# Performance work log

Hardware: AMD Instinct MI355X
Metric: run time of the kernel (lower is better)

Reference implementation:

```python
import jax, jax.numpy as jnp
import numpy as np

B, S, DM, H = 4, 2048, 768, 12
HD = DM // H
HEAD_Z = float(np.sqrt(HD))


def norm_layer(x, scale, bias):
    # custom normalization over last dim: (x - mean)/std * scale + bias, scalar scale/bias, no eps
    mean = x.mean(axis=2, keepdims=True)
    std = jnp.sqrt(((x - mean) ** 2).mean(axis=2, keepdims=True))
    return (x - mean) / std * scale + bias


def setup_inputs() -> dict:
    key = jax.random.key(0)
    ks = jax.random.split(key, 12)
    s = 1.0 / np.sqrt(DM)
    return {
        "base": jax.random.normal(ks[0], (B, S, DM), dtype=jnp.float32),
        "Wqkv": jax.random.normal(ks[1], (DM, 3 * DM), dtype=jnp.float32) * s,
        "bqkv": jax.random.normal(ks[2], (3 * DM,), dtype=jnp.float32) * s,
        "W1": jax.random.normal(ks[3], (DM, DM), dtype=jnp.float32) * s,
        "b1": jax.random.normal(ks[4], (DM,), dtype=jnp.float32) * s,
        "W2": jax.random.normal(ks[5], (DM, DM), dtype=jnp.float32) * s,
        "b2": jax.random.normal(ks[6], (DM,), dtype=jnp.float32) * s,
        "n1_scale": jax.random.uniform(ks[7], (1,), jnp.float32, -s, s) + 0.5,
        "n1_bias": jax.random.uniform(ks[8], (1,), jnp.float32, -s, s),
        "n2_scale": jax.random.uniform(ks[9], (1,), jnp.float32, -s, s) + 0.5,
        "n2_bias": jax.random.uniform(ks[10], (1,), jnp.float32, -s, s),
    }


def reference(base, Wqkv, bqkv, W1, b1, W2, b2, n1_scale, n1_bias, n2_scale, n2_bias):
    qkv = base @ Wqkv + bqkv                     # [B,S,3*DM]
    q, k, v = jnp.split(qkv, 3, axis=2)
    # per-head attention, vectorized over heads: the torch loop with broadcast-mul-sum
    # is mathematically softmax(QK^T/sqrt(hd)) @ V per head
    q = q.reshape(B, S, H, HD)
    k = k.reshape(B, S, H, HD)
    v = v.reshape(B, S, H, HD)
    scores = jnp.einsum('bqhd,bkhd->bhqk', q, k) / HEAD_Z  # [B,H,S,S]
    attn = jax.nn.softmax(scores, axis=-1)
    av = jnp.einsum('bhqk,bkhd->bqhd', attn, v).reshape(B, S, DM)
    hidden = norm_layer(av @ W1 + b1 + base, n1_scale, n1_bias)
    out = norm_layer(jax.nn.relu(hidden @ W2 + b2) + hidden, n2_scale, n2_bias)
    return out
```

## Files before the change

kernel.cpp:

```cpp
#include <hip/hip_runtime.h>
#include <hip/hip_bf16.h>
#include <stdint.h>

#define B_ 4
#define S_ 2048
#define DM_ 768
#define H_ 12
#define HD_ 64
#define ROWS (B_*S_)
#define QKVN (3*DM_)

typedef __attribute__((ext_vector_type(8))) short short8;
typedef __attribute__((ext_vector_type(4))) float floatx4;
typedef __attribute__((ext_vector_type(8))) unsigned short ushort8;
typedef __attribute__((ext_vector_type(4))) unsigned short ushort4v;
typedef __attribute__((ext_vector_type(4))) float float4_t;

__device__ __forceinline__ unsigned short f2b(float f) {
  union { float f; uint32_t u; } x; x.f = f;
  uint32_t r = x.u + 0x7FFFu + ((x.u >> 16) & 1u);
  return (unsigned short)(r >> 16);
}
__device__ __forceinline__ float b2f(unsigned short u) {
  union { uint32_t u; float f; } x; x.u = ((uint32_t)u) << 16; return x.f;
}
__device__ __forceinline__ uint32_t fbits(float f) {
  union { float f; uint32_t u; } x; x.f = f; return x.u;
}

__device__ __forceinline__ void load_lds16(const void* g, void* l) {
  __builtin_amdgcn_global_load_lds(
      (const __attribute__((address_space(1))) uint32_t*)g,
      (__attribute__((address_space(3))) uint32_t*)l, 16, 0, 0);
}

#define CVT_B 6144
#define WQ_B 1728
#define W1_B 576
__global__ __launch_bounds__(256) void prep(
    const float* __restrict__ base, unsigned short* __restrict__ base_bf,
    const float* __restrict__ Wqkv, unsigned short* __restrict__ Wqkvt,
    const float* __restrict__ W1, unsigned short* __restrict__ W1t,
    const float* __restrict__ W2, unsigned short* __restrict__ W2t) {
  __shared__ float t[32][33];
  int bid = blockIdx.x;
  int tid = threadIdx.x;
  if (bid < CVT_B) {
    int i = bid * 256 + tid;
    float4_t v = ((const float4_t*)base)[i];
    ushort4v o;
    o[0] = f2b(v[0]); o[1] = f2b(v[1]); o[2] = f2b(v[2]); o[3] = f2b(v[3]);
    ((ushort4v*)base_bf)[i] = o;
    return;
  }
  const float* W; unsigned short* Wt; int N, rel;
  if (bid < CVT_B + WQ_B)      { W = Wqkv; Wt = Wqkvt; N = QKVN; rel = bid - CVT_B; }
  else if (bid < CVT_B + WQ_B + W1_B) { W = W1; Wt = W1t; N = DM_; rel = bid - CVT_B - WQ_B; }
  else                          { W = W2; Wt = W2t; N = DM_; rel = bid - CVT_B - WQ_B - W1_B; }
  int K = DM_;
  int n0 = (rel % (N / 32)) * 32, k0 = (rel / (N / 32)) * 32;
  int tx = tid & 31, ty = tid >> 5;
#pragma unroll
  for (int i = 0; i < 4; i++)
    t[ty + i * 8][tx] = W[(size_t)(k0 + ty + i * 8) * N + n0 + tx];
  __syncthreads();
#pragma unroll
  for (int i = 0; i < 4; i++)
    Wt[(size_t)(n0 + ty + i * 8) * K + k0 + tx] = f2b(t[tx][ty + i * 8]);
}

__global__ __launch_bounds__(256, 2) void gemm_qkv(
    const unsigned short* __restrict__ A,
    const unsigned short* __restrict__ Bt,
    const float* __restrict__ bias,
    unsigned short* __restrict__ Cout,
    unsigned short* __restrict__ Vt,
    int M, int N, int K) {
  __shared__ __align__(16) unsigned short LDSbuf[2 * 128 * 128];
  unsigned short* As = LDSbuf;
  unsigned short* Bs = LDSbuf + 128 * 128;
  int tid = threadIdx.x;
  int wave = tid >> 6, lane = tid & 63;
  int quad = lane >> 4, l16 = lane & 15;
  int sr4 = lane >> 4;
  int c16 = lane & 15;
  int flat = blockIdx.x;
  int xcd = flat & 7, widx = flat >> 3;
  int mb = xcd * 8 + (widx & 7);
  int nb = widx >> 3;
  int m0 = mb * 128, n0 = nb * 128;
  int wm = (wave >> 1) * 64, wn = (wave & 1) * 64;
  floatx4 acc[4][4] = {};

  for (int kb = 0; kb < K; kb += 128) {
#pragma unroll
    for (int i = 0; i < 8; i++) {
      int op = wave * 8 + i;
      int srow = op * 4 + sr4;
      int sc = c16 ^ (srow & 15);
      load_lds16(A + (size_t)(m0 + srow) * K + kb + sc * 8, (char*)As + op * 1024);
    }
#pragma unroll
    for (int i = 0; i < 8; i++) {
      int op = wave * 8 + i;
      int srow = op * 4 + sr4;
      int sc = c16 ^ (srow & 15);
      load_lds16(Bt + (size_t)(n0 + srow) * K + kb + sc * 8, (char*)Bs + op * 1024);
    }
    __syncthreads();
#pragma unroll
    for (int ks = 0; ks < 4; ks++) {
      short8 af[4], bfr[4];
#pragma unroll
      for (int mt = 0; mt < 4; mt++)
        af[mt] = *(const short8*)(As + (wm + mt * 16 + l16) * 128 + ((ks * 4 + quad) ^ l16) * 8);
#pragma unroll
      for (int nt = 0; nt < 4; nt++)
        bfr[nt] = *(const short8*)(Bs + (wn + nt * 16 + l16) * 128 + ((ks * 4 + quad) ^ l16) * 8);
#pragma unroll
      for (int mt = 0; mt < 4; mt++)
#pragma unroll
        for (int nt = 0; nt < 4; nt++)
          acc[mt][nt] = __builtin_amdgcn_mfma_f32_16x16x32_bf16(af[mt], bfr[nt], acc[mt][nt], 0, 0, 0);
    }
    __syncthreads();
  }

  if (n0 < 2 * DM_) {
#pragma unroll
    for (int mt = 0; mt < 4; mt++) {
#pragma unroll
      for (int nt = 0; nt < 4; nt++) {
#pragma unroll
        for (int r = 0; r < 4; r++) {
          int row = m0 + wm + mt * 16 + quad * 4 + r;
          int col = n0 + wn + nt * 16 + l16;
          float v = acc[mt][nt][r] + bias[col];
          if (col < DM_) v *= 0.18033688011112042f;
          Cout[(size_t)row * N + col] = f2b(v);
        }
      }
    }
  } else {
    unsigned short* scr = LDSbuf + wave * 4608;
    int h = (n0 + wn - 2 * DM_) >> 6;
    int b = m0 >> 11;
    int s_base = (m0 & (S_ - 1)) + wm;
#pragma unroll
    for (int nt = 0; nt < 4; nt++) {
      float bv = bias[n0 + wn + nt * 16 + l16];
      ushort8 v0, v1;
#pragma unroll
      for (int j = 0; j < 8; j++) {
        v0[j] = f2b(acc[j & 3][nt][j >> 2] + bv);
        v1[j] = f2b(acc[j & 3][nt][2 + (j >> 2)] + bv);
      }
      *(ushort8*)(scr + (nt * 16 + l16) * 72 + quad * 16) = v0;
      *(ushort8*)(scr + (nt * 16 + l16) * 72 + quad * 16 + 8) = v1;
    }
#pragma unroll
    for (int it = 0; it < 8; it++) {
      int d = it * 8 + (lane >> 3);
      int ch = lane & 7;
      ushort8 w = *(const ushort8*)(scr + d * 72 + ch * 8);
      *(ushort8*)(Vt + ((size_t)(b * H_ + h) * 64 + d) * S_ + s_base + ch * 8) = w;
    }
  }
}

template <int EPI>
__global__ __launch_bounds__(256, 4) void gemm64(
    const unsigned short* __restrict__ A,
    const unsigned short* __restrict__ Bt,
    const float* __restrict__ bias,
    const unsigned short* __restrict__ res,
    unsigned short* __restrict__ Cout,
    int M, int N, int K) {
  __shared__ __align__(16) unsigned short As[64 * 64];
  __shared__ __align__(16) unsigned short Bs[128 * 64];
  int tid = threadIdx.x;
  int wave = tid >> 6, lane = tid & 63;
  int quad = lane >> 4, l16 = lane & 15;
  int e = l16 & 7;
  int sr = lane >> 3;
  int sc = (lane & 7) ^ (sr & 7);
  int flat = blockIdx.x;
  int xcd = flat & 7, widx = flat >> 3;
  int mb = xcd * 16 + (widx & 15);
  int nb = widx >> 4;
  int m0 = mb * 64, n0 = nb * 128;
  int wm = (wave >> 1) * 32, wn = (wave & 1) * 64;
  floatx4 acc[2][4] = {};

  for (int kb = 0; kb < K; kb += 64) {
#pragma unroll
    for (int i = 0; i < 2; i++) {
      int op = wave * 2 + i;
      load_lds16(A + (size_t)(m0 + op * 8 + sr) * K + kb + sc * 8, (char*)As + op * 1024);
    }
#pragma unroll
    for (int i = 0; i < 4; i++) {
      int op = wave * 4 + i;
      load_lds16(Bt + (size_t)(n0 + op * 8 + sr) * K + kb + sc * 8, (char*)Bs + op * 1024);
    }
    __syncthreads();
#pragma unroll
    for (int ks = 0; ks < 2; ks++) {
      short8 af[2], bfr[4];
#pragma unroll
      for (int mt = 0; mt < 2; mt++)
        af[mt] = *(const short8*)(As + (wm + mt * 16 + l16) * 64 + ((ks * 4 + quad) ^ e) * 8);
#pragma unroll
      for (int nt = 0; nt < 4; nt++)
        bfr[nt] = *(const short8*)(Bs + (wn + nt * 16 + l16) * 64 + ((ks * 4 + quad) ^ e) * 8);
#pragma unroll
      for (int mt = 0; mt < 2; mt++)
#pragma unroll
        for (int nt = 0; nt < 4; nt++)
          acc[mt][nt] = __builtin_amdgcn_mfma_f32_16x16x32_bf16(af[mt], bfr[nt], acc[mt][nt], 0, 0, 0);
    }
    __syncthreads();
  }
#pragma unroll
  for (int mt = 0; mt < 2; mt++) {
#pragma unroll
    for (int nt = 0; nt < 4; nt++) {
#pragma unroll
      for (int r = 0; r < 4; r++) {
        int row = m0 + wm + mt * 16 + quad * 4 + r;
        int col = n0 + wn + nt * 16 + l16;
        size_t idx = (size_t)row * N + col;
        float v = acc[mt][nt][r] + bias[col];
        if (EPI == 2) v = fmaxf(v, 0.0f);
        v += b2f(res[idx]);
        Cout[idx] = f2b(v);
      }
    }
  }
}

__global__ __launch_bounds__(256, 3) void attn(
    const unsigned short* __restrict__ qkv,
    const unsigned short* __restrict__ Vt,
    unsigned short* __restrict__ av) {
  int flat = blockIdx.x;
  int widx = (flat & 7) * 96 + (flat >> 3);
  int qt = widx & 15;
  int bh = widx >> 4;
  int b = bh / H_, h = bh % H_;
  int row0 = b * S_ + qt * 128;
  __shared__ __align__(16) unsigned short Ks[2][64 * 64];
  __shared__ __align__(16) unsigned short Vs[2][64 * 64];
  __shared__ __align__(16) unsigned short Ps[4][32 * 72];
  int tid = threadIdx.x;
  int wave = tid >> 6, lane = tid & 63;
  int quad = lane >> 4, l16 = lane & 15;
  int e = l16 & 7;
  int sr = lane >> 3;
  int sc = (lane & 7) ^ (sr & 7);

#pragma unroll
  for (int i = 0; i < 4; i++) {
    load_lds16(qkv + (size_t)(row0 + wave * 32 + i * 8 + sr) * QKVN + h * HD_ + sc * 8,
               (char*)Ps[wave] + i * 1024);
  }
  const unsigned short* kp = qkv + (size_t)(b * S_ + wave * 16 + sr) * QKVN + DM_ + h * HD_ + sc * 8;
  const unsigned short* vp = Vt + ((size_t)bh * 64 + wave * 16 + sr) * S_ + sc * 8;
  auto stageKV = [&](const unsigned short* kq, const unsigned short* vq, int buf) {
#pragma unroll
    for (int i = 0; i < 2; i++) {
      load_lds16(kq + (size_t)i * 8 * QKVN, (char*)Ks[buf] + wave * 2048 + i * 1024);
      load_lds16(vq + (size_t)i * 8 * S_, (char*)Vs[buf] + wave * 2048 + i * 1024);
    }
  };
  stageKV(kp, vp, 0);

  floatx4 accO[2][4] = {};
  floatx4 accL[2] = {};
  short8 ones;
#pragma unroll
  for (int j = 0; j < 8; j++) ones[j] = (short)0x3F80;
  __syncthreads();

  short8 qf[2][2];
#pragma unroll
  for (int mf = 0; mf < 2; mf++)
#pragma unroll
    for (int ks = 0; ks < 2; ks++)
      qf[mf][ks] = *(const short8*)(Ps[wave] + (mf * 16 + l16) * 64 + ((ks * 4 + quad) ^ e) * 8);

  int cur = 0;
  for (int kt = 0; kt < 32; kt++) {
    floatx4 sv[2][4] = {};
    __builtin_amdgcn_s_setprio(1);
#pragma unroll
    for (int ks = 0; ks < 2; ks++)
#pragma unroll
      for (int nt = 0; nt < 4; nt++) {
        short8 kf = *(const short8*)(Ks[cur] + (nt * 16 + l16) * 64 + ((ks * 4 + quad) ^ e) * 8);
#pragma unroll
        for (int mf = 0; mf < 2; mf++)
          sv[mf][nt] = __builtin_amdgcn_mfma_f32_16x16x32_bf16(qf[mf][ks], kf, sv[mf][nt], 0, 0, 0);
      }
    __builtin_amdgcn_s_setprio(0);
    if (kt + 1 < 32) {
      kp += 64 * QKVN;
      vp += 64;
      stageKV(kp, vp, cur ^ 1);
    }
#pragma unroll
    for (int mf = 0; mf < 2; mf++)
#pragma unroll
      for (int r = 0; r < 4; r++) {
        uint32_t u0 = fbits(__builtin_amdgcn_exp2f(sv[mf][0][r]));
        uint32_t u1 = fbits(__builtin_amdgcn_exp2f(sv[mf][1][r]));
        uint32_t u2 = fbits(__builtin_amdgcn_exp2f(sv[mf][2][r]));
        uint32_t u3 = fbits(__builtin_amdgcn_exp2f(sv[mf][3][r]));
        uint2 val;
        val.x = __builtin_amdgcn_perm(u1, u0, 0x07060302u);
        val.y = __builtin_amdgcn_perm(u3, u2, 0x07060302u);
        *(uint2*)(&Ps[wave][(mf * 16 + quad * 4 + r) * 72 + l16 * 4]) = val;
      }
    __builtin_amdgcn_s_setprio(1);
#pragma unroll
    for (int ks = 0; ks < 2; ks++) {
      short8 pf[2];
#pragma unroll
      for (int mf = 0; mf < 2; mf++) {
        pf[mf] = *(const short8*)(Ps[wave] + (mf * 16 + l16) * 72 + ks * 32 + quad * 8);
        accL[mf] = __builtin_amdgcn_mfma_f32_16x16x32_bf16(pf[mf], ones, accL[mf], 0, 0, 0);
      }
#pragma unroll
      for (int nt = 0; nt < 4; nt++) {
        short8 vf = *(const short8*)(Vs[cur] + (nt * 16 + l16) * 64 + ((ks * 4 + quad) ^ e) * 8);
#pragma unroll
        for (int mf = 0; mf < 2; mf++)
          accO[mf][nt] = __builtin_amdgcn_mfma_f32_16x16x32_bf16(pf[mf], vf, accO[mf][nt], 0, 0, 0);
      }
    }
    __builtin_amdgcn_s_setprio(0);
    __syncthreads();
    cur ^= 1;
  }
#pragma unroll
  for (int mf = 0; mf < 2; mf++)
#pragma unroll
    for (int r = 0; r < 4; r++) {
      float inv = 1.0f / accL[mf][r];
      int row = row0 + wave * 32 + mf * 16 + quad * 4 + r;
#pragma unroll
      for (int nt = 0; nt < 4; nt++)
        av[(size_t)row * DM_ + h * HD_ + nt * 16 + l16] = f2b(accO[mf][nt][r] * inv);
    }
}

template <int WB>
__global__ __launch_bounds__(256) void normk(
    const unsigned short* __restrict__ X, const float* __restrict__ scale,
    const float* __restrict__ bias, float* __restrict__ Y,
    unsigned short* __restrict__ Ybf) {
  int row = blockIdx.x;
  const unsigned short* x = X + (size_t)row * DM_;
  int tid = threadIdx.x;
  int wave = tid >> 6, lane = tid & 63;
  float v[3];
#pragma unroll
  for (int i = 0; i < 3; i++) v[i] = b2f(x[tid + i * 256]);
  float s = v[0] + v[1] + v[2];
#pragma unroll
  for (int o = 32; o > 0; o >>= 1) s += __shfl_xor(s, o);
  __shared__ float red[4];
  if (lane == 0) red[wave] = s;
  __syncthreads();
  float mean = (red[0] + red[1] + red[2] + red[3]) * (1.0f / DM_);
  float ss = 0.0f;
#pragma unroll
  for (int i = 0; i < 3; i++) { v[i] -= mean; ss += v[i] * v[i]; }
#pragma unroll
  for (int o = 32; o > 0; o >>= 1) ss += __shfl_xor(ss, o);
  __syncthreads();
  if (lane == 0) red[wave] = ss;
  __syncthreads();
  float var = (red[0] + red[1] + red[2] + red[3]) * (1.0f / DM_);
  float rstd = rsqrtf(var);
  float sg = scale[0], bg = bias[0];
#pragma unroll
  for (int i = 0; i < 3; i++) {
    float y = v[i] * rstd * sg + bg;
    if (WB) Ybf[(size_t)row * DM_ + tid + i * 256] = f2b(y);
    else    Y[(size_t)row * DM_ + tid + i * 256] = y;
  }
}

extern "C" void kernel_launch(void* const* d_in, const int* in_sizes, int n_in,
                              void* d_out, int out_size, void* d_ws, size_t ws_size,
                              hipStream_t stream) {
  const float* base = (const float*)d_in[0];
  const float* Wqkv = (const float*)d_in[1];
  const float* bqkv = (const float*)d_in[2];
  const float* W1 = (const float*)d_in[3];
  const float* b1 = (const float*)d_in[4];
  const float* W2 = (const float*)d_in[5];
  const float* b2 = (const float*)d_in[6];
  const float* n1s = (const float*)d_in[7];
  const float* n1b = (const float*)d_in[8];
  const float* n2s = (const float*)d_in[9];
  const float* n2b = (const float*)d_in[10];
  float* out = (float*)d_out;

  char* ws = (char*)d_ws;
  size_t off = 0;
  auto alloc = [&](size_t bytes) {
    char* p = ws + off;
    off = (off + bytes + 255) & ~(size_t)255;
    return p;
  };
  unsigned short* base_bf = (unsigned short*)alloc((size_t)ROWS * DM_ * 2);
  unsigned short* Wqkvt = (unsigned short*)alloc((size_t)QKVN * DM_ * 2);
  unsigned short* W1t = (unsigned short*)alloc((size_t)DM_ * DM_ * 2);
  unsigned short* W2t = (unsigned short*)alloc((size_t)DM_ * DM_ * 2);
  unsigned short* qkvb = (unsigned short*)alloc((size_t)ROWS * QKVN * 2);
  unsigned short* Vtb = (unsigned short*)alloc((size_t)B_ * H_ * HD_ * S_ * 2);
  unsigned short* avb = (unsigned short*)alloc((size_t)ROWS * DM_ * 2);
  unsigned short* t1b = (unsigned short*)alloc((size_t)ROWS * DM_ * 2);
  unsigned short* hbf = (unsigned short*)alloc((size_t)ROWS * DM_ * 2);

  prep<<<CVT_B + WQ_B + 2 * W1_B, 256, 0, stream>>>(
      base, base_bf, Wqkv, Wqkvt, W1, W1t, W2, W2t);
  gemm_qkv<<<dim3((QKVN / 128) * (ROWS / 128)), 256, 0, stream>>>(
      base_bf, Wqkvt, bqkv, qkvb, Vtb, ROWS, QKVN, DM_);
  attn<<<dim3((S_ / 128) * (B_ * H_)), 256, 0, stream>>>(qkvb, Vtb, avb);
  gemm64<1><<<dim3((DM_ / 128) * (ROWS / 64)), 256, 0, stream>>>(
      avb, W1t, b1, base_bf, t1b, ROWS, DM_, DM_);
  normk<1><<<ROWS, 256, 0, stream>>>(t1b, n1s, n1b, nullptr, hbf);
  gemm64<2><<<dim3((DM_ / 128) * (ROWS / 64)), 256, 0, stream>>>(
      hbf, W2t, b2, hbf, t1b, ROWS, DM_, DM_);
  normk<0><<<ROWS, 256, 0, stream>>>(t1b, n2s, n2b, out, nullptr);
}
```

Baseline: 244.5 us.

## Restructure attention to 32x32x16 MFMA with register-resident P and row sums

The attention kernel switches from 16x16x32 MFMAs to 32x32x16 MFMAs and computes S^T = K·Q^T, so that each lane's exponentiated scores can be packed straight into the B operand of the PV MFMA. This removes the LDS round-trip for P and the extra MFMA against a ones vector for the row sums; the sums are now accumulated with scalar adds plus one cross-half shuffle. Q is loaded directly into registers, and a hardware packed bf16 convert replaces the manual bit tricks. The output is staged through LDS for coalesced 16-byte stores, and the QKV epilogue's V-transpose staging is reordered to use 8-byte writes. This relies on the scale already being folded into Q, and the new register layout must match the 32x32 operand mapping exactly.

```diff
diff --git a/kernel.cpp b/kernel.cpp
--- a/kernel.cpp
+++ b/kernel.cpp
@@ -12,9 +12,11 @@
 
 typedef __attribute__((ext_vector_type(8))) short short8;
 typedef __attribute__((ext_vector_type(4))) float floatx4;
+typedef __attribute__((ext_vector_type(16))) float floatx16;
 typedef __attribute__((ext_vector_type(8))) unsigned short ushort8;
 typedef __attribute__((ext_vector_type(4))) unsigned short ushort4v;
 typedef __attribute__((ext_vector_type(4))) float float4_t;
+typedef __attribute__((ext_vector_type(4))) unsigned int uintx4;
 
 __device__ __forceinline__ unsigned short f2b(float f) {
   union { float f; uint32_t u; } x; x.f = f;
@@ -24,14 +26,16 @@
 __device__ __forceinline__ float b2f(unsigned short u) {
   union { uint32_t u; float f; } x; x.u = ((uint32_t)u) << 16; return x.f;
 }
-__device__ __forceinline__ uint32_t fbits(float f) {
-  union { float f; uint32_t u; } x; x.f = f; return x.u;
-}
 
 __device__ __forceinline__ void load_lds16(const void* g, void* l) {
   __builtin_amdgcn_global_load_lds(
       (const __attribute__((address_space(1))) uint32_t*)g,
       (__attribute__((address_space(3))) uint32_t*)l, 16, 0, 0);
+}
+__device__ __forceinline__ uint32_t cvt_pk_bf16(float a, float b) {
+  uint32_t w;
+  asm("v_cvt_pk_bf16_f32 %0, %1, %2" : "=v"(w) : "v"(a), "v"(b));
+  return w;
 }
 
 #define CVT_B 6144
@@ -146,17 +150,17 @@
     int h = (n0 + wn - 2 * DM_) >> 6;
     int b = m0 >> 11;
     int s_base = (m0 & (S_ - 1)) + wm;
+    int posq = (quad & 1) * 8 + (quad >> 1) * 4;
 #pragma unroll
     for (int nt = 0; nt < 4; nt++) {
       float bv = bias[n0 + wn + nt * 16 + l16];
-      ushort8 v0, v1;
-#pragma unroll
-      for (int j = 0; j < 8; j++) {
-        v0[j] = f2b(acc[j & 3][nt][j >> 2] + bv);
-        v1[j] = f2b(acc[j & 3][nt][2 + (j >> 2)] + bv);
+#pragma unroll
+      for (int mt = 0; mt < 4; mt++) {
+        ushort4v v;
+#pragma unroll
+        for (int r = 0; r < 4; r++) v[r] = f2b(acc[mt][nt][r] + bv);
+        *(ushort4v*)(scr + (nt * 16 + l16) * 72 + mt * 16 + posq) = v;
       }
-      *(ushort8*)(scr + (nt * 16 + l16) * 72 + quad * 16) = v0;
-      *(ushort8*)(scr + (nt * 16 + l16) * 72 + quad * 16 + 8) = v1;
     }
 #pragma unroll
     for (int it = 0; it < 8; it++) {
@@ -249,109 +253,109 @@
   int bh = widx >> 4;
   int b = bh / H_, h = bh % H_;
   int row0 = b * S_ + qt * 128;
-  __shared__ __align__(16) unsigned short Ks[2][64 * 64];
-  __shared__ __align__(16) unsigned short Vs[2][64 * 64];
-  __shared__ __align__(16) unsigned short Ps[4][32 * 72];
+  __shared__ __align__(16) unsigned short SH[4 * 64 * 64];
   int tid = threadIdx.x;
   int wave = tid >> 6, lane = tid & 63;
-  int quad = lane >> 4, l16 = lane & 15;
-  int e = l16 & 7;
+  int q = lane & 31, hi = lane >> 5;
+  int e8 = lane & 7;
   int sr = lane >> 3;
   int sc = (lane & 7) ^ (sr & 7);
 
-#pragma unroll
-  for (int i = 0; i < 4; i++) {
-    load_lds16(qkv + (size_t)(row0 + wave * 32 + i * 8 + sr) * QKVN + h * HD_ + sc * 8,
-               (char*)Ps[wave] + i * 1024);
-  }
+  const unsigned short* qrow =
+      qkv + (size_t)(row0 + wave * 32 + q) * QKVN + h * HD_ + hi * 8;
+  short8 qf[4];
+#pragma unroll
+  for (int slot = 0; slot < 4; slot++)
+    qf[slot] = *(const short8*)(qrow + slot * 16);
+
   const unsigned short* kp = qkv + (size_t)(b * S_ + wave * 16 + sr) * QKVN + DM_ + h * HD_ + sc * 8;
   const unsigned short* vp = Vt + ((size_t)bh * 64 + wave * 16 + sr) * S_ + sc * 8;
   auto stageKV = [&](const unsigned short* kq, const unsigned short* vq, int buf) {
 #pragma unroll
     for (int i = 0; i < 2; i++) {
-      load_lds16(kq + (size_t)i * 8 * QKVN, (char*)Ks[buf] + wave * 2048 + i * 1024);
-      load_lds16(vq + (size_t)i * 8 * S_, (char*)Vs[buf] + wave * 2048 + i * 1024);
+      load_lds16(kq + (size_t)i * 8 * QKVN, (char*)SH + buf * 8192 + wave * 2048 + i * 1024);
+      load_lds16(vq + (size_t)i * 8 * S_, (char*)SH + 16384 + buf * 8192 + wave * 2048 + i * 1024);
     }
   };
   stageKV(kp, vp, 0);
 
-  floatx4 accO[2][4] = {};
-  floatx4 accL[2] = {};
-  short8 ones;
-#pragma unroll
-  for (int j = 0; j < 8; j++) ones[j] = (short)0x3F80;
+  floatx16 accO[2] = {};
+  float accL = 0.0f;
   __syncthreads();
-
-  short8 qf[2][2];
-#pragma unroll
-  for (int mf = 0; mf < 2; mf++)
-#pragma unroll
-    for (int ks = 0; ks < 2; ks++)
-      qf[mf][ks] = *(const short8*)(Ps[wave] + (mf * 16 + l16) * 64 + ((ks * 4 + quad) ^ e) * 8);
 
   int cur = 0;
   for (int kt = 0; kt < 32; kt++) {
-    floatx4 sv[2][4] = {};
+    const unsigned short* Ksc = SH + cur * 4096;
+    const unsigned short* Vsc = SH + 16384 / 2 + cur * 4096;
+    floatx16 sv0 = {}, sv1 = {};
     __builtin_amdgcn_s_setprio(1);
 #pragma unroll
-    for (int ks = 0; ks < 2; ks++)
-#pragma unroll
-      for (int nt = 0; nt < 4; nt++) {
-        short8 kf = *(const short8*)(Ks[cur] + (nt * 16 + l16) * 64 + ((ks * 4 + quad) ^ e) * 8);
-#pragma unroll
-        for (int mf = 0; mf < 2; mf++)
-          sv[mf][nt] = __builtin_amdgcn_mfma_f32_16x16x32_bf16(qf[mf][ks], kf, sv[mf][nt], 0, 0, 0);
-      }
+    for (int slot = 0; slot < 4; slot++) {
+      short8 kf0 = *(const short8*)(Ksc + (q) * 64 + ((slot * 2 + hi) ^ e8) * 8);
+      short8 kf1 = *(const short8*)(Ksc + (32 + q) * 64 + ((slot * 2 + hi) ^ e8) * 8);
+      sv0 = __builtin_amdgcn_mfma_f32_32x32x16_bf16(kf0, qf[slot], sv0, 0, 0, 0);
+      sv1 = __builtin_amdgcn_mfma_f32_32x32x16_bf16(kf1, qf[slot], sv1, 0, 0, 0);
+    }
     __builtin_amdgcn_s_setprio(0);
     if (kt + 1 < 32) {
       kp += 64 * QKVN;
       vp += 64;
       stageKV(kp, vp, cur ^ 1);
     }
-#pragma unroll
-    for (int mf = 0; mf < 2; mf++)
-#pragma unroll
-      for (int r = 0; r < 4; r++) {
-        uint32_t u0 = fbits(__builtin_amdgcn_exp2f(sv[mf][0][r]));
-        uint32_t u1 = fbits(__builtin_amdgcn_exp2f(sv[mf][1][r]));
-        uint32_t u2 = fbits(__builtin_amdgcn_exp2f(sv[mf][2][r]));
-        uint32_t u3 = fbits(__builtin_amdgcn_exp2f(sv[mf][3][r]));
-        uint2 val;
-        val.x = __builtin_amdgcn_perm(u1, u0, 0x07060302u);
-        val.y = __builtin_amdgcn_perm(u3, u2, 0x07060302u);
-        *(uint2*)(&Ps[wave][(mf * 16 + quad * 4 + r) * 72 + l16 * 4]) = val;
+    uint32_t pw[4][4];
+    float psum = 0.0f;
+#pragma unroll
+    for (int s = 0; s < 4; s++) {
+#pragma unroll
+      for (int j4 = 0; j4 < 4; j4++) {
+        float a, bb;
+        if (s < 2) {
+          a = __builtin_amdgcn_exp2f(sv0[(s & 1) * 8 + 2 * j4]);
+          bb = __builtin_amdgcn_exp2f(sv0[(s & 1) * 8 + 2 * j4 + 1]);
+        } else {
+          a = __builtin_amdgcn_exp2f(sv1[(s & 1) * 8 + 2 * j4]);
+          bb = __builtin_amdgcn_exp2f(sv1[(s & 1) * 8 + 2 * j4 + 1]);
+        }
+        psum += a + bb;
+        pw[s][j4] = cvt_pk_bf16(a, bb);
       }
+    }
+    accL += psum;
     __builtin_amdgcn_s_setprio(1);
 #pragma unroll
-    for (int ks = 0; ks < 2; ks++) {
-      short8 pf[2];
-#pragma unroll
-      for (int mf = 0; mf < 2; mf++) {
-        pf[mf] = *(const short8*)(Ps[wave] + (mf * 16 + l16) * 72 + ks * 32 + quad * 8);
-        accL[mf] = __builtin_amdgcn_mfma_f32_16x16x32_bf16(pf[mf], ones, accL[mf], 0, 0, 0);
-      }
-#pragma unroll
-      for (int nt = 0; nt < 4; nt++) {
-        short8 vf = *(const short8*)(Vs[cur] + (nt * 16 + l16) * 64 + ((ks * 4 + quad) ^ e) * 8);
-#pragma unroll
-        for (int mf = 0; mf < 2; mf++)
-          accO[mf][nt] = __builtin_amdgcn_mfma_f32_16x16x32_bf16(pf[mf], vf, accO[mf][nt], 0, 0, 0);
+    for (int s = 0; s < 4; s++) {
+      uintx4 pu = {pw[s][0], pw[s][1], pw[s][2], pw[s][3]};
+      short8 pf = __builtin_bit_cast(short8, pu);
+#pragma unroll
+      for (int dt = 0; dt < 2; dt++) {
+        short8 vf = *(const short8*)(Vsc + (dt * 32 + q) * 64 + ((s * 2 + hi) ^ e8) * 8);
+        accO[dt] = __builtin_amdgcn_mfma_f32_32x32x16_bf16(vf, pf, accO[dt], 0, 0, 0);
       }
     }
     __builtin_amdgcn_s_setprio(0);
     __syncthreads();
     cur ^= 1;
   }
-#pragma unroll
-  for (int mf = 0; mf < 2; mf++)
-#pragma unroll
-    for (int r = 0; r < 4; r++) {
-      float inv = 1.0f / accL[mf][r];
-      int row = row0 + wave * 32 + mf * 16 + quad * 4 + r;
-#pragma unroll
-      for (int nt = 0; nt < 4; nt++)
-        av[(size_t)row * DM_ + h * HD_ + nt * 16 + l16] = f2b(accO[mf][nt][r] * inv);
-    }
+
+  accL += __shfl_xor(accL, 32);
+  float inv = 1.0f / accL;
+  uint32_t* scr = (uint32_t*)SH + wave * 1152;
+#pragma unroll
+  for (int t = 0; t < 2; t++) {
+#pragma unroll
+    for (int i = 0; i < 8; i++) {
+      float a = accO[t][2 * i] * inv;
+      float bb = accO[t][2 * i + 1] * inv;
+      scr[q * 36 + t * 16 + 4 * (i >> 1) + (i & 1) + 2 * hi] = cvt_pk_bf16(a, bb);
+    }
+  }
+  int q2 = lane >> 1, half = lane & 1;
+#pragma unroll
+  for (int s = 0; s < 4; s++) {
+    uintx4 w = *(const uintx4*)(scr + q2 * 36 + half * 16 + s * 4);
+    *(ushort8*)(av + (size_t)(row0 + wave * 32 + q2) * DM_ + h * HD_ + half * 32 + s * 8) =
+        __builtin_bit_cast(ushort8, w);
+  }
 }
 
 template <int WB>
```

Result: no change. 246.8 us (+1.0%).
